# Kernel tuning notes

Hardware: AMD Instinct MI355X
Metric: run time of the kernel (lower is better)

## Reference

```python
import jax, jax.numpy as jnp
import numpy as np

N_NODES = 50000
N_EDGES = 800000
IN_DIM = 256
HIDDEN = 32
HEADS = 4
OUT_DIM = 2
NEG_SLOPE = 0.2  # PyG GATConv default LeakyReLU slope


def setup_inputs() -> dict:
    key = jax.random.key(0)
    ks = jax.random.split(key, 12)
    s = 0.05
    return {
        "x": jax.random.normal(ks[0], (N_NODES, IN_DIM), dtype=jnp.float32),
        "edge_index": jax.random.randint(ks[1], (2, N_EDGES), 0, N_NODES, dtype=jnp.int32),
        # conv1: in_dim -> hidden, heads=4, concat
        "W1": jax.random.normal(ks[2], (IN_DIM, HEADS * HIDDEN), dtype=jnp.float32) * s,
        "att_src1": jax.random.normal(ks[3], (HEADS, HIDDEN), dtype=jnp.float32) * s,
        "att_dst1": jax.random.normal(ks[4], (HEADS, HIDDEN), dtype=jnp.float32) * s,
        "b1": jnp.zeros((HEADS * HIDDEN,), dtype=jnp.float32),
        # conv2: heads*hidden -> hidden, heads=1, mean (concat=False)
        "W2": jax.random.normal(ks[5], (HEADS * HIDDEN, 1 * HIDDEN), dtype=jnp.float32) * s,
        "att_src2": jax.random.normal(ks[6], (1, HIDDEN), dtype=jnp.float32) * s,
        "att_dst2": jax.random.normal(ks[7], (1, HIDDEN), dtype=jnp.float32) * s,
        "b2": jnp.zeros((HIDDEN,), dtype=jnp.float32),
        # final classifier
        "lin_w": jax.random.normal(ks[8], (HIDDEN, OUT_DIM), dtype=jnp.float32) * s,
        "lin_b": jnp.zeros((OUT_DIM,), dtype=jnp.float32),
    }


def gat_conv(x, src, dst, W, att_src, att_dst, bias, concat):
    """PyG-style GATConv (v1), eval mode (no dropout), self-loops already in src/dst."""
    N = x.shape[0]
    H, C = att_src.shape
    h = (x @ W).reshape(N, H, C)                       # [N,H,C]
    a_s = jnp.sum(h * att_src, axis=-1)                # [N,H]
    a_d = jnp.sum(h * att_dst, axis=-1)                # [N,H]
    e = jax.nn.leaky_relu(a_s[src] + a_d[dst], NEG_SLOPE)  # [E,H]
    # numerically-stable softmax over edges grouped by destination node
    m = jax.ops.segment_max(e, dst, num_segments=N)    # [N,H]
    p = jnp.exp(e - m[dst])
    denom = jax.ops.segment_sum(p, dst, num_segments=N)
    alpha = p / denom[dst]                             # [E,H]
    out = jax.ops.segment_sum(alpha[:, :, None] * h[src], dst, num_segments=N)  # [N,H,C]
    out = out.reshape(N, H * C) if concat else out.mean(axis=1)
    return out + bias


def reference(x, edge_index, W1, att_src1, att_dst1, b1, W2, att_src2, att_dst2, b2, lin_w, lin_b):
    N = x.shape[0]
    loops = jnp.arange(N, dtype=edge_index.dtype)      # PyG default add_self_loops=True
    src = jnp.concatenate([edge_index[0], loops])
    dst = jnp.concatenate([edge_index[1], loops])
    h = jax.nn.elu(gat_conv(x, src, dst, W1, att_src1, att_dst1, b1, concat=True))
    h = jax.nn.elu(gat_conv(h, src, dst, W2, att_src2, att_dst2, b2, concat=False))
    return h @ lin_w + lin_b
```

## Files before the change

kernel.cpp:

```cpp
#include <hip/hip_runtime.h>

#define IN_DIM 256
#define HID 32
#define HEADS 4
#define F1 128
#define BSHIFT 9
#define MAXBUK 128

static __device__ __forceinline__ float leaky(float x){ return x > 0.f ? x : 0.2f*x; }
static __device__ __forceinline__ float elu(float x){ return x > 0.f ? x : (__expf(x) - 1.f); }

static __device__ __forceinline__ unsigned short f2bf(float f){
  unsigned int u = __float_as_uint(f);
  u += 0x7FFFu + ((u >> 16) & 1u);
  return (unsigned short)(u >> 16);
}
static __device__ __forceinline__ float bf2f(unsigned short h){
  return __uint_as_float(((unsigned int)h) << 16);
}
static __device__ __forceinline__ unsigned int pack2(unsigned short a, unsigned short b){
  return (unsigned int)a | ((unsigned int)b << 16);
}
static __device__ __forceinline__ float bflo(unsigned int u){ return __uint_as_float(u << 16); }
static __device__ __forceinline__ float bfhi(unsigned int u){ return __uint_as_float(u & 0xFFFF0000u); }

__device__ __forceinline__ int block_excl_scan(int v, int tid, int* total){
  __shared__ int ws[8];
  int lane = tid & 63, w = tid >> 6;
  int incl = v;
  #pragma unroll
  for (int d = 1; d < 64; d <<= 1){ int o = __shfl_up(incl, d); if (lane >= d) incl += o; }
  if (lane == 63) ws[w] = incl;
  __syncthreads();
  if (tid == 0){ int s = 0; for (int i = 0; i < 4; ++i){ int t = ws[i]; ws[i] = s; s += t; } ws[4] = s; }
  __syncthreads();
  *total = ws[4];
  int e = ws[w] + incl - v;
  __syncthreads();
  return e;
}

__global__ __launch_bounds__(256) void bukcnt_kernel(const int* __restrict__ dsts,
    int* __restrict__ cnt_blk, int E, int nbuk, int stride){
  __shared__ int lcnt[MAXBUK];
  int tid = threadIdx.x, blk = blockIdx.x;
  if (tid < nbuk) lcnt[tid] = 0;
  __syncthreads();
  int base = blk*2048;
  #pragma unroll
  for (int j = 0; j < 8; ++j){
    int i = base + tid + j*256;
    if (i < E) atomicAdd(&lcnt[dsts[i] >> BSHIFT], 1);
  }
  __syncthreads();
  if (tid < nbuk) cnt_blk[tid*stride + blk] = lcnt[tid];
}

__global__ __launch_bounds__(256) void bukscan1_kernel(int* __restrict__ cnt_blk,
    int* __restrict__ btot, int nchk, int stride){
  int b = blockIdx.x, tid = threadIdx.x;
  int carry = 0;
  for (int s = 0; s < nchk; s += 256){
    int i = s + tid;
    int v = (i < nchk) ? cnt_blk[b*stride + i] : 0;
    int tot; int e = block_excl_scan(v, tid, &tot);
    if (i < nchk) cnt_blk[b*stride + i] = carry + e;
    carry += tot;
  }
  if (tid == 0) btot[b] = carry;
}

__global__ __launch_bounds__(256) void bukscan2_kernel(const int* __restrict__ btot,
    int* __restrict__ bucket_base, int* __restrict__ offs, int nbuk, int Nn, int E){
  int tid = threadIdx.x;
  int v = (tid < nbuk) ? btot[tid] : 0;
  int tot; int e = block_excl_scan(v, tid, &tot);
  if (tid <= nbuk) bucket_base[tid] = e;
  if (tid == 0) offs[Nn] = E;
}

__global__ __launch_bounds__(256) void bukscat_kernel(const int* __restrict__ srcs,
    const int* __restrict__ dsts, const int* __restrict__ cnt_blk,
    const int* __restrict__ bucket_base, unsigned int* __restrict__ im,
    int E, int nbuk, int stride){
  __shared__ int lcur[MAXBUK];
  int tid = threadIdx.x, blk = blockIdx.x;
  if (tid < nbuk) lcur[tid] = bucket_base[tid] + cnt_blk[tid*stride + blk];
  __syncthreads();
  int base = blk*2048;
  #pragma unroll
  for (int j = 0; j < 8; ++j){
    int i = base + tid + j*256;
    if (i < E){
      int s = srcs[i], d = dsts[i];
      int r = atomicAdd(&lcur[d >> BSHIFT], 1);
      im[r] = (unsigned)s | (((unsigned)d & 511u) << 16);
    }
  }
}

__global__ __launch_bounds__(256) void bukfine_kernel(const unsigned int* __restrict__ im,
    const int* __restrict__ bucket_base, int* __restrict__ offs, int* __restrict__ csr, int Nn){
  __shared__ int lcnt[512], lpfx[512];
  int b = blockIdx.x, tid = threadIdx.x;
  int node0 = b << BSHIFT;
  int nn = min(512, Nn - node0);
  lcnt[tid] = 0; lcnt[tid+256] = 0;
  __syncthreads();
  int ebeg = bucket_base[b], eend = bucket_base[b+1];
  for (int i = ebeg + tid; i < eend; i += 256)
    atomicAdd(&lcnt[im[i] >> 16], 1);
  __syncthreads();
  int carry = 0;
  for (int s = 0; s < 512; s += 256){
    int v = lcnt[s + tid];
    int tot; int e = block_excl_scan(v, tid, &tot);
    lpfx[s + tid] = carry + e;
    carry += tot;
  }
  __syncthreads();
  if (tid < nn) offs[node0 + tid] = ebeg + lpfx[tid];
  if (tid + 256 < nn) offs[node0 + tid + 256] = ebeg + lpfx[tid + 256];
  lcnt[tid] = ebeg + lpfx[tid];
  lcnt[tid+256] = ebeg + lpfx[tid+256];
  __syncthreads();
  for (int i = ebeg + tid; i < eend; i += 256){
    unsigned int u = im[i];
    int pos = atomicAdd(&lcnt[u >> 16], 1);
    csr[pos] = (int)(u & 0xFFFFu);
  }
}

__global__ __launch_bounds__(256) void convw_kernel(const float* __restrict__ W1,
    unsigned short* __restrict__ Wh, unsigned short* __restrict__ Wl){
  int i = blockIdx.x*256 + threadIdx.x;
  int n = i >> 8, k = i & 255;
  float w = W1[(size_t)k*F1 + n];
  unsigned short h = f2bf(w);
  Wh[i] = h;
  Wl[i] = f2bf(w - bf2f(h));
}

typedef __attribute__((ext_vector_type(8))) short bf8_t;
typedef __attribute__((ext_vector_type(4))) float f4_t;

__global__ __launch_bounds__(256) void gemm1_kernel(const float* __restrict__ x,
    const unsigned short* __restrict__ Wh, const unsigned short* __restrict__ Wl,
    const float* __restrict__ att_src, const float* __restrict__ att_dst,
    unsigned short* __restrict__ h1b, float* __restrict__ as1, float* __restrict__ ad1, int M){
  __shared__ uint4 AhV[64][5], AlV[64][5];
  __shared__ uint4 BhV[128][5], BlV[128][5];
  const int tid = threadIdx.x;
  const int m0 = blockIdx.x*64;
  const int wave = tid >> 6, lane = tid & 63;
  const int quad = lane >> 4, l16 = lane & 15;
  const int wr = (wave & 1)*32;
  const int wc = (wave >> 1)*64;
  f4_t acc[2][4];
  #pragma unroll
  for (int r = 0; r < 2; ++r)
    #pragma unroll
    for (int c = 0; c < 4; ++c)
      #pragma unroll
      for (int i = 0; i < 4; ++i) acc[r][c][i] = 0.f;

  const int ar = tid >> 2, akc = tid & 3;
  const bool aok = (m0 + ar) < M;
  const float* ap = x + (size_t)(m0 + ar)*IN_DIM + 8*akc;
  const int bn = tid >> 1, bkc = (tid & 1)*2;
  const unsigned short* bph = Wh + (size_t)bn*256 + 16*(tid & 1);
  const unsigned short* bpl = Wl + (size_t)bn*256 + 16*(tid & 1);

  for (int k0 = 0; k0 < IN_DIM; k0 += 32){
    float4 a0 = make_float4(0.f,0.f,0.f,0.f), a1 = a0;
    if (aok){ a0 = *(const float4*)(ap + k0); a1 = *(const float4*)(ap + k0 + 4); }
    float v[8] = {a0.x,a0.y,a0.z,a0.w,a1.x,a1.y,a1.z,a1.w};
    unsigned short hh[8], ll[8];
    #pragma unroll
    for (int j = 0; j < 8; ++j){
      unsigned short h = f2bf(v[j]); hh[j] = h; ll[j] = f2bf(v[j] - bf2f(h));
    }
    uint4 hv; hv.x = pack2(hh[0],hh[1]); hv.y = pack2(hh[2],hh[3]); hv.z = pack2(hh[4],hh[5]); hv.w = pack2(hh[6],hh[7]);
    uint4 lv; lv.x = pack2(ll[0],ll[1]); lv.y = pack2(ll[2],ll[3]); lv.z = pack2(ll[4],ll[5]); lv.w = pack2(ll[6],ll[7]);
    AhV[ar][akc] = hv;
    AlV[ar][akc] = lv;
    BhV[bn][bkc+0] = *(const uint4*)(bph + k0);
    BhV[bn][bkc+1] = *(const uint4*)(bph + k0 + 8);
    BlV[bn][bkc+0] = *(const uint4*)(bpl + k0);
    BlV[bn][bkc+1] = *(const uint4*)(bpl + k0 + 8);
    __syncthreads();

    bf8_t arh[2], arl[2], brh[4], brl[4];
    #pragma unroll
    for (int r = 0; r < 2; ++r){
      arh[r] = *(const bf8_t*)&AhV[wr + r*16 + l16][quad];
      arl[r] = *(const bf8_t*)&AlV[wr + r*16 + l16][quad];
    }
    #pragma unroll
    for (int c = 0; c < 4; ++c){
      brh[c] = *(const bf8_t*)&BhV[wc + c*16 + l16][quad];
      brl[c] = *(const bf8_t*)&BlV[wc + c*16 + l16][quad];
    }
    #pragma unroll
    for (int r = 0; r < 2; ++r)
      #pragma unroll
      for (int c = 0; c < 4; ++c){
        acc[r][c] = __builtin_amdgcn_mfma_f32_16x16x32_bf16(arh[r], brh[c], acc[r][c], 0, 0, 0);
        acc[r][c] = __builtin_amdgcn_mfma_f32_16x16x32_bf16(arh[r], brl[c], acc[r][c], 0, 0, 0);
        acc[r][c] = __builtin_amdgcn_mfma_f32_16x16x32_bf16(arl[r], brh[c], acc[r][c], 0, 0, 0);
      }
    __syncthreads();
  }

  const int head0 = wc >> 5;
  float sv[4], dv[4];
  #pragma unroll
  for (int c = 0; c < 4; ++c){
    int col_in_head = (c & 1)*16 + l16;
    sv[c] = att_src[(head0 + (c >> 1))*HID + col_in_head];
    dv[c] = att_dst[(head0 + (c >> 1))*HID + col_in_head];
  }
  #pragma unroll
  for (int r = 0; r < 2; ++r){
    #pragma unroll
    for (int i = 0; i < 4; ++i){
      int row = m0 + wr + r*16 + quad*4 + i;
      bool ok = row < M;
      float hv0 = acc[r][0][i], hv1 = acc[r][1][i], hv2 = acc[r][2][i], hv3 = acc[r][3][i];
      if (ok){
        unsigned short* hp = h1b + (size_t)row*F1 + wc + l16;
        hp[0]  = f2bf(hv0); hp[16] = f2bf(hv1); hp[32] = f2bf(hv2); hp[48] = f2bf(hv3);
      }
      float p0 = hv0*sv[0] + hv1*sv[1];
      float p1 = hv2*sv[2] + hv3*sv[3];
      float q0 = hv0*dv[0] + hv1*dv[1];
      float q1 = hv2*dv[2] + hv3*dv[3];
      p0 += __shfl_xor(p0,1); p0 += __shfl_xor(p0,2); p0 += __shfl_xor(p0,4); p0 += __shfl_xor(p0,8);
      p1 += __shfl_xor(p1,1); p1 += __shfl_xor(p1,2); p1 += __shfl_xor(p1,4); p1 += __shfl_xor(p1,8);
      q0 += __shfl_xor(q0,1); q0 += __shfl_xor(q0,2); q0 += __shfl_xor(q0,4); q0 += __shfl_xor(q0,8);
      q1 += __shfl_xor(q1,1); q1 += __shfl_xor(q1,2); q1 += __shfl_xor(q1,4); q1 += __shfl_xor(q1,8);
      if (ok && l16 == 0){
        as1[row*4 + head0]     = p0;
        as1[row*4 + head0 + 1] = p1;
        ad1[row*4 + head0]     = q0;
        ad1[row*4 + head0 + 1] = q1;
      }
    }
  }
}

__global__ __launch_bounds__(256) void agg1_kernel(const unsigned int* __restrict__ h1b,
    const float* __restrict__ a_s1, const float* __restrict__ a_d1,
    const int* __restrict__ offs, const int* __restrict__ csr,
    const float* __restrict__ b1, uint4* __restrict__ h1a4, int N){
  int n = blockIdx.x*4 + (threadIdx.x >> 6);
  if (n >= N) return;
  const int lane = threadIdx.x & 63;
  const int sub  = lane >> 4;
  const int cl   = lane & 15;
  const int head = cl >> 2;
  const float ad = a_d1[n*4+head];
  const int cw = 4*cl;
  float a0=0,a1=0,a2=0,a3=0,a4=0,a5=0,a6=0,a7=0,den=0;
  if (sub == 0){
    float p = __expf(leaky(a_s1[n*4+head] + ad));
    uint4 u = *(const uint4*)(h1b + (size_t)n*64 + cw);
    a0 = p*bflo(u.x); a1 = p*bfhi(u.x); a2 = p*bflo(u.y); a3 = p*bfhi(u.y);
    a4 = p*bflo(u.z); a5 = p*bfhi(u.z); a6 = p*bflo(u.w); a7 = p*bfhi(u.w);
    den = p;
  }
  const int beg = offs[n], end = offs[n+1];
  int e = beg + sub;
  for (; e + 12 < end; e += 16){
    int s0 = csr[e], s1 = csr[e+4], s2 = csr[e+8], s3 = csr[e+12];
    float p0 = __expf(leaky(a_s1[s0*4+head] + ad));
    float p1 = __expf(leaky(a_s1[s1*4+head] + ad));
    float p2 = __expf(leaky(a_s1[s2*4+head] + ad));
    float p3 = __expf(leaky(a_s1[s3*4+head] + ad));
    uint4 u0 = *(const uint4*)(h1b + (size_t)s0*64 + cw);
    uint4 u1 = *(const uint4*)(h1b + (size_t)s1*64 + cw);
    uint4 u2 = *(const uint4*)(h1b + (size_t)s2*64 + cw);
    uint4 u3 = *(const uint4*)(h1b + (size_t)s3*64 + cw);
    a0 += p0*bflo(u0.x) + p1*bflo(u1.x) + p2*bflo(u2.x) + p3*bflo(u3.x);
    a1 += p0*bfhi(u0.x) + p1*bfhi(u1.x) + p2*bfhi(u2.x) + p3*bfhi(u3.x);
    a2 += p0*bflo(u0.y) + p1*bflo(u1.y) + p2*bflo(u2.y) + p3*bflo(u3.y);
    a3 += p0*bfhi(u0.y) + p1*bfhi(u1.y) + p2*bfhi(u2.y) + p3*bfhi(u3.y);
    a4 += p0*bflo(u0.z) + p1*bflo(u1.z) + p2*bflo(u2.z) + p3*bflo(u3.z);
    a5 += p0*bfhi(u0.z) + p1*bfhi(u1.z) + p2*bfhi(u2.z) + p3*bfhi(u3.z);
    a6 += p0*bflo(u0.w) + p1*bflo(u1.w) + p2*bflo(u2.w) + p3*bflo(u3.w);
    a7 += p0*bfhi(u0.w) + p1*bfhi(u1.w) + p2*bfhi(u2.w) + p3*bfhi(u3.w);
    den += p0 + p1 + p2 + p3;
  }
  for (; e < end; e += 4){
    int s = csr[e];
    float p = __expf(leaky(a_s1[s*4+head] + ad));
    uint4 u = *(const uint4*)(h1b + (size_t)s*64 + cw);
    a0 += p*bflo(u.x); a1 += p*bfhi(u.x); a2 += p*bflo(u.y); a3 += p*bfhi(u.y);
    a4 += p*bflo(u.z); a5 += p*bfhi(u.z); a6 += p*bflo(u.w); a7 += p*bfhi(u.w);
    den += p;
  }
  #pragma unroll
  for (int off = 16; off < 64; off <<= 1){
    a0 += __shfl_xor(a0,off); a1 += __shfl_xor(a1,off);
    a2 += __shfl_xor(a2,off); a3 += __shfl_xor(a3,off);
    a4 += __shfl_xor(a4,off); a5 += __shfl_xor(a5,off);
    a6 += __shfl_xor(a6,off); a7 += __shfl_xor(a7,off);
    den += __shfl_xor(den,off);
  }
  if (sub == 0){
    float inv = 1.f/den;
    int ch = 8*cl;
    float4 b0 = *(const float4*)(b1 + ch);
    float4 b4 = *(const float4*)(b1 + ch + 4);
    uint4 w;
    w.x = pack2(f2bf(elu(a0*inv+b0.x)), f2bf(elu(a1*inv+b0.y)));
    w.y = pack2(f2bf(elu(a2*inv+b0.z)), f2bf(elu(a3*inv+b0.w)));
    w.z = pack2(f2bf(elu(a4*inv+b4.x)), f2bf(elu(a5*inv+b4.y)));
    w.w = pack2(f2bf(elu(a6*inv+b4.z)), f2bf(elu(a7*inv+b4.w)));
    h1a4[(size_t)n*16 + cl] = w;
  }
}

__global__ __launch_bounds__(256) void gemm2_kernel(const uint4* __restrict__ h1a4, const float* __restrict__ W2,
    const float* __restrict__ att_src, const float* __restrict__ att_dst,
    unsigned int* __restrict__ h2b, float* __restrict__ as2, float* __restrict__ ad2, int M){
  __shared__ float As[64*132];
  __shared__ float Ws[128*32];
  const int tid = threadIdx.x;
  const int cg = tid & 15;
  const int rg = tid >> 4;
  const int m0 = blockIdx.x*64;
  #pragma unroll
  for (int p = 0; p < 4; ++p){
    int j = tid + 256*p;
    int r = j >> 4, q = j & 15;
    int row = m0 + r;
    uint4 u = make_uint4(0,0,0,0);
    if (row < M) u = h1a4[(size_t)row*16 + q];
    float4 f0 = make_float4(bflo(u.x), bfhi(u.x), bflo(u.y), bfhi(u.y));
    float4 f1 = make_float4(bflo(u.z), bfhi(u.z), bflo(u.w), bfhi(u.w));
    *(float4*)&As[r*132 + 8*q]     = f0;
    *(float4*)&As[r*132 + 8*q + 4] = f1;
  }
  #pragma unroll
  for (int p = 0; p < 4; ++p){
    int i = tid + 256*p;
    ((float4*)Ws)[i] = ((const float4*)W2)[i];
  }
  __syncthreads();
  float acc[4][2] = {};
  const float* a0p = &As[(4*rg+0)*132];
  const float* a1p = &As[(4*rg+1)*132];
  const float* a2p = &As[(4*rg+2)*132];
  const float* a3p = &As[(4*rg+3)*132];
  #pragma unroll 8
  for (int kk = 0; kk < 128; ++kk){
    float2 w = *(const float2*)&Ws[kk*32 + 2*cg];
    float a0 = a0p[kk], a1 = a1p[kk], a2 = a2p[kk], a3 = a3p[kk];
    acc[0][0]+=a0*w.x; acc[0][1]+=a0*w.y;
    acc[1][0]+=a1*w.x; acc[1][1]+=a1*w.y;
    acc[2][0]+=a2*w.x; acc[2][1]+=a2*w.y;
    acc[3][0]+=a3*w.x; acc[3][1]+=a3*w.y;
  }
  const float2 sv = *(const float2*)(att_src + 2*cg);
  const float2 dv = *(const float2*)(att_dst + 2*cg);
  #pragma unroll
  for (int i = 0; i < 4; ++i){
    int row = m0 + 4*rg + i;
    if (row < M){
      float2 o = make_float2(acc[i][0], acc[i][1]);
      h2b[(size_t)row*16 + cg] = pack2(f2bf(o.x), f2bf(o.y));
      float ps = o.x*sv.x + o.y*sv.y;
      float pd = o.x*dv.x + o.y*dv.y;
      ps += __shfl_xor(ps,1); ps += __shfl_xor(ps,2); ps += __shfl_xor(ps,4); ps += __shfl_xor(ps,8);
      pd += __shfl_xor(pd,1); pd += __shfl_xor(pd,2); pd += __shfl_xor(pd,4); pd += __shfl_xor(pd,8);
      if (cg == 0){ as2[row] = ps; ad2[row] = pd; }
    }
  }
}

__global__ __launch_bounds__(256) void agg2_kernel(const unsigned int* __restrict__ h2b,
    const float* __restrict__ as2, const float* __restrict__ ad2,
    const int* __restrict__ offs, const int* __restrict__ csr,
    const float* __restrict__ b2, const float* __restrict__ linw, const float* __restrict__ linb,
    float* __restrict__ out, int N){
  int n = blockIdx.x*4 + (threadIdx.x >> 6);
  if (n >= N) return;
  const int lane = threadIdx.x & 63;
  const int sub  = lane >> 3;
  const int cl   = lane & 7;
  const int cw   = 2*cl;
  const float ad = ad2[n];
  float a0=0,a1=0,a2=0,a3=0,den=0;
  if (sub == 0){
    float p = __expf(leaky(as2[n] + ad));
    uint2 u = *(const uint2*)(h2b + (size_t)n*16 + cw);
    a0 = p*bflo(u.x); a1 = p*bfhi(u.x); a2 = p*bflo(u.y); a3 = p*bfhi(u.y);
    den = p;
  }
  const int beg = offs[n], end = offs[n+1];
  int e = beg + sub;
  for (; e + 24 < end; e += 32){
    int s0 = csr[e], s1 = csr[e+8], s2 = csr[e+16], s3 = csr[e+24];
    float p0 = __expf(leaky(as2[s0] + ad));
    float p1 = __expf(leaky(as2[s1] + ad));
    float p2 = __expf(leaky(as2[s2] + ad));
    float p3 = __expf(leaky(as2[s3] + ad));
    uint2 u0 = *(const uint2*)(h2b + (size_t)s0*16 + cw);
    uint2 u1 = *(const uint2*)(h2b + (size_t)s1*16 + cw);
    uint2 u2 = *(const uint2*)(h2b + (size_t)s2*16 + cw);
    uint2 u3 = *(const uint2*)(h2b + (size_t)s3*16 + cw);
    a0 += p0*bflo(u0.x) + p1*bflo(u1.x) + p2*bflo(u2.x) + p3*bflo(u3.x);
    a1 += p0*bfhi(u0.x) + p1*bfhi(u1.x) + p2*bfhi(u2.x) + p3*bfhi(u3.x);
    a2 += p0*bflo(u0.y) + p1*bflo(u1.y) + p2*bflo(u2.y) + p3*bflo(u3.y);
    a3 += p0*bfhi(u0.y) + p1*bfhi(u1.y) + p2*bfhi(u2.y) + p3*bfhi(u3.y);
    den += p0 + p1 + p2 + p3;
  }
  for (; e < end; e += 8){
    int s = csr[e];
    float p = __expf(leaky(as2[s] + ad));
    uint2 u = *(const uint2*)(h2b + (size_t)s*16 + cw);
    a0 += p*bflo(u.x); a1 += p*bfhi(u.x); a2 += p*bflo(u.y); a3 += p*bfhi(u.y);
    den += p;
  }
  #pragma unroll
  for (int off = 8; off < 64; off <<= 1){
    a0 += __shfl_xor(a0,off); a1 += __shfl_xor(a1,off);
    a2 += __shfl_xor(a2,off); a3 += __shfl_xor(a3,off);
    den += __shfl_xor(den,off);
  }
  float inv = 1.f/den;
  int ch = 4*cl;
  float o0 = elu(a0*inv + b2[ch+0]);
  float o1 = elu(a1*inv + b2[ch+1]);
  float o2 = elu(a2*inv + b2[ch+2]);
  float o3 = elu(a3*inv + b2[ch+3]);
  float r0 = o0*linw[2*(ch+0)]   + o1*linw[2*(ch+1)]   + o2*linw[2*(ch+2)]   + o3*linw[2*(ch+3)];
  float r1 = o0*linw[2*(ch+0)+1] + o1*linw[2*(ch+1)+1] + o2*linw[2*(ch+2)+1] + o3*linw[2*(ch+3)+1];
  r0 += __shfl_xor(r0,1); r0 += __shfl_xor(r0,2); r0 += __shfl_xor(r0,4);
  r1 += __shfl_xor(r1,1); r1 += __shfl_xor(r1,2); r1 += __shfl_xor(r1,4);
  if (lane == 0){
    out[(size_t)n*2+0] = r0 + linb[0];
    out[(size_t)n*2+1] = r1 + linb[1];
  }
}

extern "C" void kernel_launch(void* const* d_in, const int* in_sizes, int n_in,
                              void* d_out, int out_size, void* d_ws, size_t ws_size,
                              hipStream_t stream) {
  const float* x    = (const float*)d_in[0];
  const int*   ei   = (const int*)  d_in[1];
  const float* W1   = (const float*)d_in[2];
  const float* as1w = (const float*)d_in[3];
  const float* ad1w = (const float*)d_in[4];
  const float* b1   = (const float*)d_in[5];
  const float* W2   = (const float*)d_in[6];
  const float* as2w = (const float*)d_in[7];
  const float* ad2w = (const float*)d_in[8];
  const float* b2   = (const float*)d_in[9];
  const float* linw = (const float*)d_in[10];
  const float* linb = (const float*)d_in[11];
  float* out = (float*)d_out;

  const int N = in_sizes[0] / IN_DIM;
  const int E = in_sizes[1] / 2;

  const int NBUK = (N + 511) >> BSHIFT;
  const int NCHK = (E + 2047) / 2048;
  const int CSTR = (NCHK + 3) & ~3;

  char* ws = (char*)d_ws;
  auto alloc = [&](size_t bytes) -> char* {
    char* p = ws; ws += (bytes + 255) & ~(size_t)255; return p;
  };
  unsigned short* h1b = (unsigned short*)alloc((size_t)N*F1*2);
  uint4* h1a4 = (uint4*)alloc((size_t)N*F1*2);
  unsigned int* h2b = (unsigned int*)alloc((size_t)N*HID*2);
  float* a_s1 = (float*)alloc((size_t)N*4*4);
  float* a_d1 = (float*)alloc((size_t)N*4*4);
  float* a_s2 = (float*)alloc((size_t)N*4);
  float* a_d2 = (float*)alloc((size_t)N*4);
  size_t cntblk_bytes = (size_t)NBUK*CSTR*4;
  if (cntblk_bytes < 131072) cntblk_bytes = 131072;
  int* cnt_blk = (int*)alloc(cntblk_bytes);
  int* btot    = (int*)alloc((size_t)(NBUK+1)*4);
  int* bbase   = (int*)alloc((size_t)(NBUK+1)*4);
  int* offs    = (int*)alloc((size_t)(N+1)*4);
  int* csr     = (int*)alloc((size_t)E*4);
  unsigned int* im = (unsigned int*)h1b;
  unsigned short* W1h = (unsigned short*)cnt_blk;
  unsigned short* W1l = W1h + (size_t)IN_DIM*F1;

  const int* srcs = ei;
  const int* dsts = ei + E;

  bukcnt_kernel<<<NCHK, 256, 0, stream>>>(dsts, cnt_blk, E, NBUK, CSTR);
  bukscan1_kernel<<<NBUK, 256, 0, stream>>>(cnt_blk, btot, NCHK, CSTR);
  bukscan2_kernel<<<1, 256, 0, stream>>>(btot, bbase, offs, NBUK, N, E);
  bukscat_kernel<<<NCHK, 256, 0, stream>>>(srcs, dsts, cnt_blk, bbase, im, E, NBUK, CSTR);
  bukfine_kernel<<<NBUK, 256, 0, stream>>>(im, bbase, offs, csr, N);
  convw_kernel<<<(IN_DIM*F1)/256, 256, 0, stream>>>(W1, W1h, W1l);
  gemm1_kernel<<<(N+63)/64, 256, 0, stream>>>(x, W1h, W1l, as1w, ad1w, h1b, a_s1, a_d1, N);
  agg1_kernel<<<(N+3)/4, 256, 0, stream>>>((const unsigned int*)h1b, a_s1, a_d1, offs, csr, b1, h1a4, N);
  gemm2_kernel<<<(N+63)/64, 256, 0, stream>>>(h1a4, W2, as2w, ad2w, h2b, a_s2, a_d2, N);
  agg2_kernel<<<(N+3)/4, 256, 0, stream>>>(h2b, a_s2, a_d2, offs, csr, b2, linw, linb, out, N);
}
```

Measured before the change: 244.0 us.

## Switch intermediates from bf16 to fp16 and share edge exp weights via shuffles

Stores the layer-1 and layer-2 intermediate features as fp16 instead of bf16, using hardware half conversions, which gives more mantissa precision at the same storage size. In both aggregation kernels, each group of lanes that shares a head now computes one exp per lane for one of four edges and broadcasts it with shuffles, instead of every lane computing all four exps and gathering four attention scores. This cuts redundant transcendental work and score loads but adds cross-lane shuffle traffic. fp16 also risks overflow if feature magnitudes grow large.

Result: no change. 242.8 us (-0.5%).

```diff
diff --git a/kernel.cpp b/kernel.cpp
--- a/kernel.cpp
+++ b/kernel.cpp
@@ -1,4 +1,5 @@
 #include <hip/hip_runtime.h>
+#include <hip/hip_fp16.h>
 
 #define IN_DIM 256
 #define HID 32
@@ -21,8 +22,15 @@
 static __device__ __forceinline__ unsigned int pack2(unsigned short a, unsigned short b){
   return (unsigned int)a | ((unsigned int)b << 16);
 }
-static __device__ __forceinline__ float bflo(unsigned int u){ return __uint_as_float(u << 16); }
-static __device__ __forceinline__ float bfhi(unsigned int u){ return __uint_as_float(u & 0xFFFF0000u); }
+static __device__ __forceinline__ unsigned short f2h(float f){
+  return __half_as_ushort(__float2half(f));
+}
+static __device__ __forceinline__ float hlo(unsigned int u){
+  return __half2float(__ushort_as_half((unsigned short)(u & 0xFFFFu)));
+}
+static __device__ __forceinline__ float hhi(unsigned int u){
+  return __half2float(__ushort_as_half((unsigned short)(u >> 16)));
+}
 
 __device__ __forceinline__ int block_excl_scan(int v, int tid, int* total){
   __shared__ int ws[8];
@@ -229,7 +237,7 @@
       float hv0 = acc[r][0][i], hv1 = acc[r][1][i], hv2 = acc[r][2][i], hv3 = acc[r][3][i];
       if (ok){
         unsigned short* hp = h1b + (size_t)row*F1 + wc + l16;
-        hp[0]  = f2bf(hv0); hp[16] = f2bf(hv1); hp[32] = f2bf(hv2); hp[48] = f2bf(hv3);
+        hp[0]  = f2h(hv0); hp[16] = f2h(hv1); hp[32] = f2h(hv2); hp[48] = f2h(hv3);
       }
       float p0 = hv0*sv[0] + hv1*sv[1];
       float p1 = hv2*sv[2] + hv3*sv[3];
@@ -259,44 +267,48 @@
   const int sub  = lane >> 4;
   const int cl   = lane & 15;
   const int head = cl >> 2;
+  const int j    = cl & 3;
+  const int pbase = (lane & ~15) + (head << 2);
   const float ad = a_d1[n*4+head];
   const int cw = 4*cl;
   float a0=0,a1=0,a2=0,a3=0,a4=0,a5=0,a6=0,a7=0,den=0;
   if (sub == 0){
     float p = __expf(leaky(a_s1[n*4+head] + ad));
     uint4 u = *(const uint4*)(h1b + (size_t)n*64 + cw);
-    a0 = p*bflo(u.x); a1 = p*bfhi(u.x); a2 = p*bflo(u.y); a3 = p*bfhi(u.y);
-    a4 = p*bflo(u.z); a5 = p*bfhi(u.z); a6 = p*bflo(u.w); a7 = p*bfhi(u.w);
+    a0 = p*hlo(u.x); a1 = p*hhi(u.x); a2 = p*hlo(u.y); a3 = p*hhi(u.y);
+    a4 = p*hlo(u.z); a5 = p*hhi(u.z); a6 = p*hlo(u.w); a7 = p*hhi(u.w);
     den = p;
   }
   const int beg = offs[n], end = offs[n+1];
   int e = beg + sub;
   for (; e + 12 < end; e += 16){
     int s0 = csr[e], s1 = csr[e+4], s2 = csr[e+8], s3 = csr[e+12];
-    float p0 = __expf(leaky(a_s1[s0*4+head] + ad));
-    float p1 = __expf(leaky(a_s1[s1*4+head] + ad));
-    float p2 = __expf(leaky(a_s1[s2*4+head] + ad));
-    float p3 = __expf(leaky(a_s1[s3*4+head] + ad));
+    int sown = j == 0 ? s0 : (j == 1 ? s1 : (j == 2 ? s2 : s3));
+    float pown = __expf(leaky(a_s1[sown*4+head] + ad));
+    float p0 = __shfl(pown, pbase+0);
+    float p1 = __shfl(pown, pbase+1);
+    float p2 = __shfl(pown, pbase+2);
+    float p3 = __shfl(pown, pbase+3);
     uint4 u0 = *(const uint4*)(h1b + (size_t)s0*64 + cw);
     uint4 u1 = *(const uint4*)(h1b + (size_t)s1*64 + cw);
     uint4 u2 = *(const uint4*)(h1b + (size_t)s2*64 + cw);
     uint4 u3 = *(const uint4*)(h1b + (size_t)s3*64 + cw);
-    a0 += p0*bflo(u0.x) + p1*bflo(u1.x) + p2*bflo(u2.x) + p3*bflo(u3.x);
-    a1 += p0*bfhi(u0.x) + p1*bfhi(u1.x) + p2*bfhi(u2.x) + p3*bfhi(u3.x);
-    a2 += p0*bflo(u0.y) + p1*bflo(u1.y) + p2*bflo(u2.y) + p3*bflo(u3.y);
-    a3 += p0*bfhi(u0.y) + p1*bfhi(u1.y) + p2*bfhi(u2.y) + p3*bfhi(u3.y);
-    a4 += p0*bflo(u0.z) + p1*bflo(u1.z) + p2*bflo(u2.z) + p3*bflo(u3.z);
-    a5 += p0*bfhi(u0.z) + p1*bfhi(u1.z) + p2*bfhi(u2.z) + p3*bfhi(u3.z);
-    a6 += p0*bflo(u0.w) + p1*bflo(u1.w) + p2*bflo(u2.w) + p3*bflo(u3.w);
-    a7 += p0*bfhi(u0.w) + p1*bfhi(u1.w) + p2*bfhi(u2.w) + p3*bfhi(u3.w);
+    a0 += p0*hlo(u0.x) + p1*hlo(u1.x) + p2*hlo(u2.x) + p3*hlo(u3.x);
+    a1 += p0*hhi(u0.x) + p1*hhi(u1.x) + p2*hhi(u2.x) + p3*hhi(u3.x);
+    a2 += p0*hlo(u0.y) + p1*hlo(u1.y) + p2*hlo(u2.y) + p3*hlo(u3.y);
+    a3 += p0*hhi(u0.y) + p1*hhi(u1.y) + p2*hhi(u2.y) + p3*hhi(u3.y);
+    a4 += p0*hlo(u0.z) + p1*hlo(u1.z) + p2*hlo(u2.z) + p3*hlo(u3.z);
+    a5 += p0*hhi(u0.z) + p1*hhi(u1.z) + p2*hhi(u2.z) + p3*hhi(u3.z);
+    a6 += p0*hlo(u0.w) + p1*hlo(u1.w) + p2*hlo(u2.w) + p3*hlo(u3.w);
+    a7 += p0*hhi(u0.w) + p1*hhi(u1.w) + p2*hhi(u2.w) + p3*hhi(u3.w);
     den += p0 + p1 + p2 + p3;
   }
   for (; e < end; e += 4){
     int s = csr[e];
     float p = __expf(leaky(a_s1[s*4+head] + ad));
     uint4 u = *(const uint4*)(h1b + (size_t)s*64 + cw);
-    a0 += p*bflo(u.x); a1 += p*bfhi(u.x); a2 += p*bflo(u.y); a3 += p*bfhi(u.y);
-    a4 += p*bflo(u.z); a5 += p*bfhi(u.z); a6 += p*bflo(u.w); a7 += p*bfhi(u.w);
+    a0 += p*hlo(u.x); a1 += p*hhi(u.x); a2 += p*hlo(u.y); a3 += p*hhi(u.y);
+    a4 += p*hlo(u.z); a5 += p*hhi(u.z); a6 += p*hlo(u.w); a7 += p*hhi(u.w);
     den += p;
   }
   #pragma unroll
@@ -313,10 +325,10 @@
     float4 b0 = *(const float4*)(b1 + ch);
     float4 b4 = *(const float4*)(b1 + ch + 4);
     uint4 w;
-    w.x = pack2(f2bf(elu(a0*inv+b0.x)), f2bf(elu(a1*inv+b0.y)));
-    w.y = pack2(f2bf(elu(a2*inv+b0.z)), f2bf(elu(a3*inv+b0.w)));
-    w.z = pack2(f2bf(elu(a4*inv+b4.x)), f2bf(elu(a5*inv+b4.y)));
-    w.w = pack2(f2bf(elu(a6*inv+b4.z)), f2bf(elu(a7*inv+b4.w)));
+    w.x = pack2(f2h(elu(a0*inv+b0.x)), f2h(elu(a1*inv+b0.y)));
+    w.y = pack2(f2h(elu(a2*inv+b0.z)), f2h(elu(a3*inv+b0.w)));
+    w.z = pack2(f2h(elu(a4*inv+b4.x)), f2h(elu(a5*inv+b4.y)));
+    w.w = pack2(f2h(elu(a6*inv+b4.z)), f2h(elu(a7*inv+b4.w)));
     h1a4[(size_t)n*16 + cl] = w;
   }
 }
@@ -332,13 +344,13 @@
   const int m0 = blockIdx.x*64;
   #pragma unroll
   for (int p = 0; p < 4; ++p){
-    int j = tid + 256*p;
-    int r = j >> 4, q = j & 15;
+    int jj = tid + 256*p;
+    int r = jj >> 4, q = jj & 15;
     int row = m0 + r;
     uint4 u = make_uint4(0,0,0,0);
     if (row < M) u = h1a4[(size_t)row*16 + q];
-    float4 f0 = make_float4(bflo(u.x), bfhi(u.x), bflo(u.y), bfhi(u.y));
-    float4 f1 = make_float4(bflo(u.z), bfhi(u.z), bflo(u.w), bfhi(u.w));
+    float4 f0 = make_float4(hlo(u.x), hhi(u.x), hlo(u.y), hhi(u.y));
+    float4 f1 = make_float4(hlo(u.z), hhi(u.z), hlo(u.w), hhi(u.w));
     *(float4*)&As[r*132 + 8*q]     = f0;
     *(float4*)&As[r*132 + 8*q + 4] = f1;
   }
@@ -369,7 +381,7 @@
     int row = m0 + 4*rg + i;
     if (row < M){
       float2 o = make_float2(acc[i][0], acc[i][1]);
-      h2b[(size_t)row*16 + cg] = pack2(f2bf(o.x), f2bf(o.y));
+      h2b[(size_t)row*16 + cg] = pack2(f2h(o.x), f2h(o.y));
       float ps = o.x*sv.x + o.y*sv.y;
       float pd = o.x*dv.x + o.y*dv.y;
       ps += __shfl_xor(ps,1); ps += __shfl_xor(ps,2); ps += __shfl_xor(ps,4); ps += __shfl_xor(ps,8);
@@ -389,38 +401,42 @@
   const int lane = threadIdx.x & 63;
   const int sub  = lane >> 3;
   const int cl   = lane & 7;
+  const int j    = cl & 3;
+  const int pbase = lane & ~7;
   const int cw   = 2*cl;
   const float ad = ad2[n];
   float a0=0,a1=0,a2=0,a3=0,den=0;
   if (sub == 0){
     float p = __expf(leaky(as2[n] + ad));
     uint2 u = *(const uint2*)(h2b + (size_t)n*16 + cw);
-    a0 = p*bflo(u.x); a1 = p*bfhi(u.x); a2 = p*bflo(u.y); a3 = p*bfhi(u.y);
+    a0 = p*hlo(u.x); a1 = p*hhi(u.x); a2 = p*hlo(u.y); a3 = p*hhi(u.y);
     den = p;
   }
   const int beg = offs[n], end = offs[n+1];
   int e = beg + sub;
   for (; e + 24 < end; e += 32){
     int s0 = csr[e], s1 = csr[e+8], s2 = csr[e+16], s3 = csr[e+24];
-    float p0 = __expf(leaky(as2[s0] + ad));
-    float p1 = __expf(leaky(as2[s1] + ad));
-    float p2 = __expf(leaky(as2[s2] + ad));
-    float p3 = __expf(leaky(as2[s3] + ad));
+    int sown = j == 0 ? s0 : (j == 1 ? s1 : (j == 2 ? s2 : s3));
+    float pown = __expf(leaky(as2[sown] + ad));
+    float p0 = __shfl(pown, pbase+0);
+    float p1 = __shfl(pown, pbase+1);
+    float p2 = __shfl(pown, pbase+2);
+    float p3 = __shfl(pown, pbase+3);
     uint2 u0 = *(const uint2*)(h2b + (size_t)s0*16 + cw);
     uint2 u1 = *(const uint2*)(h2b + (size_t)s1*16 + cw);
     uint2 u2 = *(const uint2*)(h2b + (size_t)s2*16 + cw);
     uint2 u3 = *(const uint2*)(h2b + (size_t)s3*16 + cw);
-    a0 += p0*bflo(u0.x) + p1*bflo(u1.x) + p2*bflo(u2.x) + p3*bflo(u3.x);
-    a1 += p0*bfhi(u0.x) + p1*bfhi(u1.x) + p2*bfhi(u2.x) + p3*bfhi(u3.x);
-    a2 += p0*bflo(u0.y) + p1*bflo(u1.y) + p2*bflo(u2.y) + p3*bflo(u3.y);
-    a3 += p0*bfhi(u0.y) + p1*bfhi(u1.y) + p2*bfhi(u2.y) + p3*bfhi(u3.y);
+    a0 += p0*hlo(u0.x) + p1*hlo(u1.x) + p2*hlo(u2.x) + p3*hlo(u3.x);
+    a1 += p0*hhi(u0.x) + p1*hhi(u1.x) + p2*hhi(u2.x) + p3*hhi(u3.x);
+    a2 += p0*hlo(u0.y) + p1*hlo(u1.y) + p2*hlo(u2.y) + p3*hlo(u3.y);
+    a3 += p0*hhi(u0.y) + p1*hhi(u1.y) + p2*hhi(u2.y) + p3*hhi(u3.y);
     den += p0 + p1 + p2 + p3;
   }
   for (; e < end; e += 8){
     int s = csr[e];
     float p = __expf(leaky(as2[s] + ad));
     uint2 u = *(const uint2*)(h2b + (size_t)s*16 + cw);
-    a0 += p*bflo(u.x); a1 += p*bfhi(u.x); a2 += p*bflo(u.y); a3 += p*bfhi(u.y);
+    a0 += p*hlo(u.x); a1 += p*hhi(u.x); a2 += p*hlo(u.y); a3 += p*hhi(u.y);
     den += p;
   }
   #pragma unroll
```
